# Optimization experiments

Hardware: AMD Instinct MI355X
Metric: run time of the kernel (lower is better)

## Reference

```python
import jax, jax.numpy as jnp
import numpy as np
import math

NUM_HEAD = 4
GROUPS = 32
EPS = 1e-5


def setup_inputs() -> dict:
    key = jax.random.key(0)
    k1, k2, k3 = jax.random.split(key, 3)
    B, C, H, W = 2, 256, 64, 64
    x = jax.random.normal(k1, (B, C, H, W), dtype=jnp.float32)
    gn_w = jnp.ones((C,), dtype=jnp.float32)
    gn_b = jnp.zeros((C,), dtype=jnp.float32)
    # scaling_init 'u' with scale=1: bound = sqrt(3*2/(fan_in+fan_out))
    fan = (C + 3 * C) / 2
    bound_qkv = math.sqrt(3.0 / fan)
    qkv_w = jax.random.uniform(k2, (3 * C, C), dtype=jnp.float32, minval=-bound_qkv, maxval=bound_qkv)
    bound_o = math.sqrt(3e-10 / C)
    o_w = jax.random.uniform(k3, (C, C), dtype=jnp.float32, minval=-bound_o, maxval=bound_o)
    o_b = jnp.zeros((C,), dtype=jnp.float32)
    return {"x": x, "gn_w": gn_w, "gn_b": gn_b, "qkv_w": qkv_w, "o_w": o_w, "o_b": o_b}


def _group_norm(x, w, b):
    B, C, H, W = x.shape
    xg = x.reshape(B, GROUPS, C // GROUPS, H, W)
    mean = xg.mean(axis=(2, 3, 4), keepdims=True)
    var = xg.var(axis=(2, 3, 4), keepdims=True)
    xn = ((xg - mean) * jax.lax.rsqrt(var + EPS)).reshape(B, C, H, W)
    return xn * w[None, :, None, None] + b[None, :, None, None]


def reference(x, gn_w, gn_b, qkv_w, o_w, o_b):
    B, C, H, W = x.shape
    hd = C // NUM_HEAD
    S = H * W
    norm = _group_norm(x, gn_w, gn_b)
    # 1x1 conv (no bias) == channel matmul
    qkv = jnp.einsum('oc,bchw->bohw', qkv_w, norm)
    qkv = qkv.reshape(B, NUM_HEAD, 3 * hd, S)
    q, k, v = jnp.split(qkv, 3, axis=2)  # each [B, nh, hd, S]
    scale = 1.0 / math.sqrt(C)  # note: sqrt(C), not sqrt(head_dim), per source
    attn = jnp.einsum('bncs,bnct->bnst', q, k) * scale  # [B, nh, S, S]
    attn = jax.nn.softmax(attn, axis=-1)
    out = jnp.einsum('bnst,bnct->bncs', attn, v).reshape(B, C, H, W)
    out = jnp.einsum('oc,bchw->bohw', o_w, out) + o_b[None, :, None, None]
    return out + x
```

## Files before the change

kernel.cpp:

```cpp
#include <hip/hip_runtime.h>
#include <hip/hip_bf16.h>

typedef __hip_bfloat16 bf16;
typedef short short8 __attribute__((ext_vector_type(8)));
typedef float f32x4 __attribute__((ext_vector_type(4)));

__device__ __forceinline__ float b2f(bf16 v) { return __bfloat162float(v); }

__device__ __forceinline__ unsigned short f2bf(float x) {
  unsigned u = __builtin_bit_cast(unsigned, x);
  unsigned r = u + 0x7fffu + ((u >> 16) & 1u);
  return (unsigned short)(r >> 16);
}
__device__ __forceinline__ unsigned pk2(float a, float b) {
  return (unsigned)f2bf(a) | ((unsigned)f2bf(b) << 16);
}
__device__ __forceinline__ unsigned pk2t(float a, float b) {
  return __builtin_amdgcn_perm(__builtin_bit_cast(unsigned, b),
                               __builtin_bit_cast(unsigned, a), 0x07060302u);
}
__device__ __forceinline__ float rd(const void* p, size_t i, int is32) {
  return is32 ? ((const float*)p)[i] : b2f(((const bf16*)p)[i]);
}
__device__ __forceinline__ float blo(unsigned w) {
  return __builtin_bit_cast(float, w << 16);
}
__device__ __forceinline__ float bhi(unsigned w) {
  return __builtin_bit_cast(float, w & 0xffff0000u);
}
__device__ __forceinline__ float fexp2(float x) {
  return __builtin_amdgcn_exp2f(x);
}

#define CQ 0.09016844005556022f

__global__ void __launch_bounds__(256) detect_kernel(const void* __restrict__ x,
                                                     int* __restrict__ flag) {
  __shared__ int cnt[256];
  const bf16* xb = (const bf16*)x;
  int c = 0;
  for (int i = threadIdx.x; i < 4096; i += 256) {
    float v = fabsf(b2f(xb[2 * i]));
    if (v >= 0.0009765625f && v <= 1024.0f) c++;
  }
  cnt[threadIdx.x] = c;
  __syncthreads();
  for (int off = 128; off > 0; off >>= 1) {
    if (threadIdx.x < off) cnt[threadIdx.x] += cnt[threadIdx.x + off];
    __syncthreads();
  }
  if (threadIdx.x == 0) *flag = (cnt[0] < 2048) ? 1 : 0;
}

__global__ void __launch_bounds__(256) pre1_kernel(
    const void* __restrict__ x, const void* __restrict__ gn_w,
    const void* __restrict__ gn_b, const int* __restrict__ flag,
    float* __restrict__ scale, float* __restrict__ shift,
    short* __restrict__ xT) {
  __shared__ __align__(16) float F[64][72];
  const int t = threadIdx.x;
  const int is32 = *flag;
  if (blockIdx.x < 512) {
    const int bx = blockIdx.x;
    const int b = bx >> 8, rest = bx & 255;
    const int s0 = (rest >> 2) * 64, c0 = (rest & 3) * 64;
    if (is32) {
      const float* xp = (const float*)x;
#pragma unroll
      for (int k = 0; k < 4; k++) {
        int idx = k * 256 + t, cl = idx >> 4, c4 = idx & 15;
        float4 v = *(const float4*)&xp[(size_t)(b * 256 + c0 + cl) * 4096 + s0 +
                                       c4 * 4];
        *(float4*)&F[cl][c4 * 4] = v;
      }
    } else {
      const bf16* xp = (const bf16*)x;
#pragma unroll
      for (int k = 0; k < 2; k++) {
        int idx = k * 256 + t, cl = idx >> 3, c8 = idx & 7;
        uint4 u = *(const uint4*)&xp[(size_t)(b * 256 + c0 + cl) * 4096 + s0 +
                                     c8 * 8];
        float4 f0, f1;
        f0.x = blo(u.x); f0.y = bhi(u.x); f0.z = blo(u.y); f0.w = bhi(u.y);
        f1.x = blo(u.z); f1.y = bhi(u.z); f1.z = blo(u.w); f1.w = bhi(u.w);
        *(float4*)&F[cl][c8 * 8] = f0;
        *(float4*)&F[cl][c8 * 8 + 4] = f1;
      }
    }
    __syncthreads();
#pragma unroll
    for (int k = 0; k < 8; k++) {
      int idx = k * 256 + t;
      int sl = idx >> 5, c2 = (idx & 31) * 2;
      unsigned u = pk2(F[c2][sl], F[c2 + 1][sl]);
      *(unsigned*)&xT[((size_t)b * 4096 + s0 + sl) * 256 + c0 + c2] = u;
    }
  } else {
    const int idx0 = blockIdx.x - 512;
    const int b = idx0 >> 5, g = idx0 & 31;
    const size_t base = (size_t)(b * 256 + g * 8) * 4096;
    float s = 0.f, ss = 0.f;
    if (is32) {
      const float4* p = (const float4*)((const float*)x + base);
      for (int i = t; i < 8192; i += 256) {
        float4 v = p[i];
        s += (v.x + v.y) + (v.z + v.w);
        ss += v.x * v.x + v.y * v.y + v.z * v.z + v.w * v.w;
      }
    } else {
      const uint4* p = (const uint4*)((const bf16*)x + base);
      for (int i = t; i < 4096; i += 256) {
        uint4 u = p[i];
#pragma unroll
        for (int k = 0; k < 4; k++) {
          unsigned w = (&u.x)[k];
          float lo = blo(w), hi = bhi(w);
          s += lo + hi;
          ss += lo * lo + hi * hi;
        }
      }
    }
    float* rs = &F[0][0];
    float* rq = rs + 256;
    rs[t] = s;
    rq[t] = ss;
    __syncthreads();
    for (int off = 128; off > 0; off >>= 1) {
      if (t < off) {
        rs[t] += rs[t + off];
        rq[t] += rq[t + off];
      }
      __syncthreads();
    }
    if (t < 8) {
      const float inv_n = 1.f / 32768.f;
      float mean = rs[0] * inv_n;
      float var = rq[0] * inv_n - mean * mean;
      float rstd = rsqrtf(var + 1e-5f);
      int c = g * 8 + t;
      float sc = rd(gn_w, c, is32) * rstd;
      scale[b * 256 + c] = sc;
      shift[b * 256 + c] = rd(gn_b, c, is32) - mean * sc;
    }
  }
}

__global__ void __launch_bounds__(256) pre2_kernel(
    const void* __restrict__ qkv_w, const void* __restrict__ o_w,
    const void* __restrict__ o_b, const float* __restrict__ scale,
    const float* __restrict__ shift, const int* __restrict__ flag,
    short* __restrict__ W2, float* __restrict__ bias2, short* __restrict__ owb,
    float* __restrict__ obf) {
  const int is32 = *flag;
  if (blockIdx.x < 192) {
    const int b = blockIdx.y;
    const int o = blockIdx.x * 4 + (threadIdx.x >> 6);
    const int lane = threadIdx.x & 63;
    const float f = (o % 192 < 64) ? CQ : 1.0f;
    float w[4], acc = 0.f;
#pragma unroll
    for (int k = 0; k < 4; k++) {
      int c = lane * 4 + k;
      w[k] = rd(qkv_w, (size_t)o * 256 + c, is32);
      acc += w[k] * shift[b * 256 + c];
      w[k] = w[k] * scale[b * 256 + c] * f;
    }
#pragma unroll
    for (int m = 1; m < 64; m <<= 1) acc += __shfl_xor(acc, m);
    if (lane == 0) bias2[b * 768 + o] = acc * f;
    uint2 u;
    u.x = pk2(w[0], w[1]);
    u.y = pk2(w[2], w[3]);
    *(uint2*)&W2[((size_t)b * 768 + o) * 256 + lane * 4] = u;
  } else if (blockIdx.y == 0) {
    int bx = blockIdx.x - 192;
    int i = (bx * 256 + threadIdx.x) * 4;
    uint2 u;
    u.x = pk2(rd(o_w, i, is32), rd(o_w, i + 1, is32));
    u.y = pk2(rd(o_w, i + 2, is32), rd(o_w, i + 3, is32));
    *(uint2*)&owb[i] = u;
    if (bx == 0) obf[threadIdx.x] = rd(o_b, threadIdx.x, is32);
  }
}

__global__ void __launch_bounds__(256) gemm_qkv_kernel(
    const short* __restrict__ xT, const short* __restrict__ W2,
    const float* __restrict__ bias2, short* __restrict__ qT,
    short* __restrict__ kF, short* __restrict__ vF) {
  __shared__ __align__(16) short lds[128 * 72 + 64 * 72];
  short* At = lds;
  short* Bt = lds + 128 * 72;
  const int t = threadIdx.x;
  const int wave = t >> 6, lane = t & 63;
  const int ln = lane & 15, quad = lane >> 4;
  const int s0 = blockIdx.x * 128, by = blockIdx.y, b = blockIdx.z;
  const int o0 = by * 64;
  const short* xg = xT + ((size_t)b * 4096 + s0) * 256;
  const short* wg = W2 + ((size_t)b * 768 + o0) * 256;

  f32x4 acc[2][4];
#pragma unroll
  for (int mt = 0; mt < 2; mt++)
#pragma unroll
    for (int nt = 0; nt < 4; nt++) {
      f32x4 z = {0.f, 0.f, 0.f, 0.f};
      acc[mt][nt] = z;
    }

  for (int kt = 0; kt < 4; kt++) {
    __syncthreads();
    {
      int r = t >> 1, ch = t & 1;
#pragma unroll
      for (int j = 0; j < 4; j++)
        *(uint4*)&At[r * 72 + ch * 32 + j * 8] =
            *(const uint4*)&xg[(size_t)r * 256 + kt * 64 + ch * 32 + j * 8];
    }
    {
      int r = t >> 2, cq = t & 3;
#pragma unroll
      for (int j = 0; j < 2; j++)
        *(uint4*)&Bt[r * 72 + cq * 16 + j * 8] =
            *(const uint4*)&wg[(size_t)r * 256 + kt * 64 + cq * 16 + j * 8];
    }
    __syncthreads();
#pragma unroll
    for (int kd = 0; kd < 2; kd++) {
      short8 a[2], bb[4];
#pragma unroll
      for (int mt = 0; mt < 2; mt++)
        a[mt] = *(const short8*)&At[(wave * 32 + mt * 16 + ln) * 72 + kd * 32 +
                                    quad * 8];
#pragma unroll
      for (int nt = 0; nt < 4; nt++)
        bb[nt] = *(const short8*)&Bt[(nt * 16 + ln) * 72 + kd * 32 + quad * 8];
#pragma unroll
      for (int mt = 0; mt < 2; mt++)
#pragma unroll
        for (int nt = 0; nt < 4; nt++)
          acc[mt][nt] = __builtin_amdgcn_mfma_f32_16x16x32_bf16(
              a[mt], bb[nt], acc[mt][nt], 0, 0, 0);
    }
  }

  const int h = by / 3, seg = by % 3;
  const size_t bh = (size_t)b * 4 + h;
  __syncthreads();
  if (seg != 2) {
    short* T = At;
#pragma unroll
    for (int mt = 0; mt < 2; mt++)
#pragma unroll
      for (int nt = 0; nt < 4; nt++)
#pragma unroll
        for (int r = 0; r < 4; r++)
          T[(wave * 32 + mt * 16 + quad * 4 + r) * 72 + nt * 16 + ln] =
              (short)f2bf(acc[mt][nt][r] + bias2[b * 768 + o0 + nt * 16 + ln]);
    __syncthreads();
    if (seg == 0) {
      short* dst = qT + (bh * 4096 + s0) * 64;
      int r = t >> 1, ch = t & 1;
#pragma unroll
      for (int j = 0; j < 2; j++)
        *(uint4*)&dst[r * 64 + ch * 32 + j * 8] =
            *(const uint4*)&T[r * 72 + ch * 32 + j * 8];
    } else {
      short* dstf = kF + bh * 262144;
#pragma unroll
      for (int c = 0; c < 4; c++) {
        int cid = wave * 4 + c;
        int tile = cid >> 1, kd = cid & 1;
        short8 v =
            *(const short8*)&T[(tile * 16 + ln) * 72 + kd * 32 + quad * 8];
        *(short8*)&dstf[(size_t)((s0 / 16 + tile) * 2 + kd) * 512 + lane * 8] =
            v;
      }
    }
  } else {
    short* T2 = At;
#pragma unroll
    for (int mt = 0; mt < 2; mt++)
#pragma unroll
      for (int nt = 0; nt < 4; nt++) {
        float bv = bias2[b * 768 + o0 + nt * 16 + ln];
        uint2 u;
        u.x = pk2(acc[mt][nt][0] + bv, acc[mt][nt][1] + bv);
        u.y = pk2(acc[mt][nt][2] + bv, acc[mt][nt][3] + bv);
        *(uint2*)&T2[(nt * 16 + ln) * 132 + wave * 32 + mt * 16 + quad * 4] = u;
      }
    __syncthreads();
    short* dstf = vF + bh * 262144;
#pragma unroll
    for (int c = 0; c < 4; c++) {
      int cid = wave * 4 + c;
      int ktl = cid >> 3, rem = cid & 7, dt = rem >> 1, kc = rem & 1;
      short8 v = *(const short8*)&T2[(dt * 16 + ln) * 132 + ktl * 64 + kc * 32 +
                                     quad * 8];
      *(short8*)&dstf[(size_t)(((s0 / 64 + ktl) * 4 + dt) * 2 + kc) * 512 +
                      lane * 8] = v;
    }
  }
}

__global__ void __launch_bounds__(256, 4) flash_kernel(
    const short* __restrict__ qT, const short* __restrict__ kF,
    const short* __restrict__ vF, short* __restrict__ attT) {
  __shared__ float smem[4 * 64 * 20];
  const int t = threadIdx.x;
  const int wave = t >> 6, lane = t & 63;
  const int ln = lane & 15, quad = lane >> 4;
  const int L = blockIdx.x;
  const int bh = L & 7;
  const int b = bh >> 2, h = bh & 3;
  const int q0 = (L >> 3) * 32;
  const int qt_sel = wave & 1;
  const int half = wave >> 1;

  const short* qg = qT + ((size_t)bh * 4096 + q0 + qt_sel * 16) * 64;
  const short* kf = kF + (size_t)bh * 262144 + (size_t)half * 131072;
  const short* vf = vF + (size_t)bh * 262144 + (size_t)half * 131072;

  short8 qf[2];
#pragma unroll
  for (int kd = 0; kd < 2; kd++)
    qf[kd] = *(const short8*)&qg[ln * 64 + kd * 32 + quad * 8];

  f32x4 ot[4];
#pragma unroll
  for (int dt = 0; dt < 4; dt++) {
    f32x4 z = {0.f, 0.f, 0.f, 0.f};
    ot[dt] = z;
  }
  float lres = 0.f;

  auto LOADKV = [&](short8(&ka)[2][2], short8(&va)[4], int it) {
    const short* kb = kf + (size_t)(it * 2) * 1024;
#pragma unroll
    for (int ct = 0; ct < 2; ct++)
#pragma unroll
      for (int kd = 0; kd < 2; kd++)
        ka[ct][kd] = *(const short8*)&kb[(ct * 2 + kd) * 512 + lane * 8];
    const short* vb = vf + (size_t)(it >> 1) * 4096;
    const int kc = it & 1;
#pragma unroll
    for (int dt = 0; dt < 4; dt++)
      va[dt] = *(const short8*)&vb[(dt * 2 + kc) * 512 + lane * 8];
  };

  auto STEP = [&](const short8(&ka)[2][2], const short8(&va)[4]) {
    f32x4 st[2];
#pragma unroll
    for (int ct = 0; ct < 2; ct++) {
      f32x4 z = {0.f, 0.f, 0.f, 0.f};
      st[ct] = z;
    }
#pragma unroll
    for (int kd = 0; kd < 2; kd++)
#pragma unroll
      for (int ct = 0; ct < 2; ct++)
        st[ct] = __builtin_amdgcn_mfma_f32_16x16x32_bf16(ka[ct][kd], qf[kd],
                                                         st[ct], 0, 0, 0);
    unsigned pk[2][2];
#pragma unroll
    for (int ct = 0; ct < 2; ct++) {
      float p0 = fexp2(st[ct][0]);
      float p1 = fexp2(st[ct][1]);
      float p2 = fexp2(st[ct][2]);
      float p3 = fexp2(st[ct][3]);
      lres += (p0 + p1) + (p2 + p3);
      pk[ct][0] = pk2t(p0, p1);
      pk[ct][1] = pk2t(p2, p3);
    }
    const int tt = quad >> 1;
    const int qs = (quad & 1) * 2;
    union {
      unsigned u[4];
      short8 s;
    } bu;
    bu.u[0] = (unsigned)__shfl((int)pk[tt][0], qs * 16 + ln);
    bu.u[1] = (unsigned)__shfl((int)pk[tt][1], qs * 16 + ln);
    bu.u[2] = (unsigned)__shfl((int)pk[tt][0], (qs + 1) * 16 + ln);
    bu.u[3] = (unsigned)__shfl((int)pk[tt][1], (qs + 1) * 16 + ln);
#pragma unroll
    for (int dt = 0; dt < 4; dt++)
      ot[dt] = __builtin_amdgcn_mfma_f32_16x16x32_bf16(va[dt], bu.s, ot[dt], 0,
                                                       0, 0);
  };

  short8 kaA[2][2], vaA[4], kaB[2][2], vaB[4];
  LOADKV(kaA, vaA, 0);
#pragma unroll 1
  for (int it = 0; it < 64; it += 2) {
    LOADKV(kaB, vaB, it + 1);
    STEP(kaA, vaA);
    if (it < 62) LOADKV(kaA, vaA, it + 2);
    STEP(kaB, vaB);
  }

  lres += __shfl_xor(lres, 16);
  lres += __shfl_xor(lres, 32);
  float* my = smem + (wave * 64 + lane) * 20;
#pragma unroll
  for (int dt = 0; dt < 4; dt++) *(f32x4*)&my[dt * 4] = ot[dt];
  my[16] = lres;
  __syncthreads();

  {
    const float* pA = smem + ((wave & 1) * 64 + lane) * 20;
    const float* pB = smem + (((wave & 1) + 2) * 64 + lane) * 20;
    float lf = pA[16] + pB[16];
    float invl = 1.f / lf;
    int s = q0 + (wave & 1) * 16 + ln;
    short* ap = attT + ((size_t)b * 4096 + s) * 256 + h * 64;
#pragma unroll
    for (int j = 0; j < 2; j++) {
      int dt = (wave >> 1) * 2 + j;
      f32x4 oA = *(const f32x4*)&pA[dt * 4];
      f32x4 oB = *(const f32x4*)&pB[dt * 4];
      uint2 u;
      u.x = pk2((oA[0] + oB[0]) * invl, (oA[1] + oB[1]) * invl);
      u.y = pk2((oA[2] + oB[2]) * invl, (oA[3] + oB[3]) * invl);
      *(uint2*)&ap[dt * 16 + quad * 4] = u;
    }
  }
}

__global__ void __launch_bounds__(256) gemm_o_kernel(
    const short* __restrict__ owb, const short* __restrict__ attT,
    const float* __restrict__ obf, const void* __restrict__ xres,
    void* __restrict__ out, const int* __restrict__ flag) {
  __shared__ __align__(16) float ldsf[64 * 66];
  short* Bt = (short*)ldsf;
  short* At = Bt + 64 * 72;
  const int t = threadIdx.x;
  const int wave = t >> 6, lane = t & 63;
  const int ln = lane & 15, quad = lane >> 4;
  const int s0 = blockIdx.x * 64, o0 = blockIdx.y * 64, b = blockIdx.z;
  const short* ag = attT + ((size_t)b * 4096 + s0) * 256;

  f32x4 acc[4];
#pragma unroll
  for (int mt = 0; mt < 4; mt++) {
    f32x4 z = {0.f, 0.f, 0.f, 0.f};
    acc[mt] = z;
  }

  for (int kt = 0; kt < 4; kt++) {
    __syncthreads();
    {
      int r = t >> 2, cq = t & 3;
#pragma unroll
      for (int j = 0; j < 2; j++)
        *(uint4*)&Bt[r * 72 + cq * 16 + j * 8] =
            *(const uint4*)&ag[(size_t)r * 256 + kt * 64 + cq * 16 + j * 8];
    }
    {
      int r = t >> 2, cq = t & 3;
#pragma unroll
      for (int j = 0; j < 2; j++)
        *(uint4*)&At[r * 72 + cq * 16 + j * 8] =
            *(const uint4*)&owb[(size_t)(o0 + r) * 256 + kt * 64 + cq * 16 +
                                j * 8];
    }
    __syncthreads();
#pragma unroll
    for (int kd = 0; kd < 2; kd++) {
      short8 a[4];
#pragma unroll
      for (int mt = 0; mt < 4; mt++)
        a[mt] = *(const short8*)&At[(mt * 16 + ln) * 72 + kd * 32 + quad * 8];
      short8 bb =
          *(const short8*)&Bt[(wave * 16 + ln) * 72 + kd * 32 + quad * 8];
#pragma unroll
      for (int mt = 0; mt < 4; mt++)
        acc[mt] = __builtin_amdgcn_mfma_f32_16x16x32_bf16(a[mt], bb, acc[mt],
                                                          0, 0, 0);
    }
  }

  __syncthreads();
#pragma unroll
  for (int mt = 0; mt < 4; mt++)
#pragma unroll
    for (int r = 0; r < 4; r++)
      ldsf[(mt * 16 + quad * 4 + r) * 66 + wave * 16 + ln] = acc[mt][r];
  __syncthreads();

  const int is32 = *flag;
#pragma unroll
  for (int j = 0; j < 4; j++) {
    int ol = j * 16 + (t >> 4);
    int sl = (t & 15) * 4;
    f32x4 v = *(const f32x4*)&ldsf[ol * 66 + sl];
    int o = o0 + ol;
    float bv = obf[o];
    size_t base = ((size_t)b * 256 + o) * 4096 + s0 + sl;
    if (is32) {
      const float4 rr = *(const float4*)&((const float*)xres)[base];
      float4 w;
      w.x = v[0] + bv + rr.x;
      w.y = v[1] + bv + rr.y;
      w.z = v[2] + bv + rr.z;
      w.w = v[3] + bv + rr.w;
      *(float4*)&((float*)out)[base] = w;
    } else {
      const uint2 rr = *(const uint2*)&((const bf16*)xres)[base];
      uint2 w;
      w.x = pk2(v[0] + bv + blo(rr.x), v[1] + bv + bhi(rr.x));
      w.y = pk2(v[2] + bv + blo(rr.y), v[3] + bv + bhi(rr.y));
      *(uint2*)&((bf16*)out)[base] = w;
    }
  }
}

extern "C" void kernel_launch(void* const* d_in, const int* in_sizes, int n_in,
                              void* d_out, int out_size, void* d_ws,
                              size_t ws_size, hipStream_t stream) {
  float* ws = (float*)d_ws;
  int* flag = (int*)ws;
  float* scale = ws + 256;
  float* shift = ws + 768;
  float* bias2 = ws + 1280;
  float* obf = ws + 2816;
  short* owb = (short*)(ws + 3072);
  short* W2 = (short*)(ws + 35840);
  short* xT = (short*)(ws + 232448);
  short* qT = (short*)(ws + 1281024);
  short* kF = (short*)(ws + 2329600);
  short* vF = (short*)(ws + 3378176);
  short* attT = (short*)(ws + 4426752);

  detect_kernel<<<1, 256, 0, stream>>>(d_in[0], flag);
  pre1_kernel<<<576, 256, 0, stream>>>(d_in[0], d_in[1], d_in[2], flag, scale,
                                       shift, xT);
  pre2_kernel<<<dim3(256, 2), 256, 0, stream>>>(d_in[3], d_in[4], d_in[5],
                                                scale, shift, flag, W2, bias2,
                                                owb, obf);
  gemm_qkv_kernel<<<dim3(32, 12, 2), 256, 0, stream>>>(xT, W2, bias2, qT, kF,
                                                       vF);
  flash_kernel<<<1024, 256, 0, stream>>>(qT, kF, vF, attT);
  gemm_o_kernel<<<dim3(64, 4, 2), 256, 0, stream>>>(owb, attT, obf, d_in[0],
                                                    d_out, flag);
}
```

Baseline: 172.7 us.

## Split KV across all four waves and reuse each K/V fragment for two query tiles

Each wave now handles both 16-row query tiles and a quarter of the key sequence, where before it handled one query tile and half the keys. Every loaded K/V fragment feeds two query tiles, which halves global K/V traffic per block and gives more MFMA work per load. The cost is more accumulator registers, a larger shared-memory reduction buffer (8 partial slices) and a four-way final combine, which may reduce occupancy at the launch bound of 4 blocks.

After: 161.1 us (median of 2 runs). -6.7%, faster.

```diff
diff --git a/kernel.cpp b/kernel.cpp
--- a/kernel.cpp
+++ b/kernel.cpp
@@ -305,7 +305,7 @@
 __global__ void __launch_bounds__(256, 4) flash_kernel(
     const short* __restrict__ qT, const short* __restrict__ kF,
     const short* __restrict__ vF, short* __restrict__ attT) {
-  __shared__ float smem[4 * 64 * 20];
+  __shared__ float smem[8 * 64 * 20];
   const int t = threadIdx.x;
   const int wave = t >> 6, lane = t & 63;
   const int ln = lane & 15, quad = lane >> 4;
@@ -313,33 +313,37 @@
   const int bh = L & 7;
   const int b = bh >> 2, h = bh & 3;
   const int q0 = (L >> 3) * 32;
-  const int qt_sel = wave & 1;
-  const int half = wave >> 1;
-
-  const short* qg = qT + ((size_t)bh * 4096 + q0 + qt_sel * 16) * 64;
-  const short* kf = kF + (size_t)bh * 262144 + (size_t)half * 131072;
-  const short* vf = vF + (size_t)bh * 262144 + (size_t)half * 131072;
-
-  short8 qf[2];
-#pragma unroll
-  for (int kd = 0; kd < 2; kd++)
-    qf[kd] = *(const short8*)&qg[ln * 64 + kd * 32 + quad * 8];
-
-  f32x4 ot[4];
-#pragma unroll
-  for (int dt = 0; dt < 4; dt++) {
-    f32x4 z = {0.f, 0.f, 0.f, 0.f};
-    ot[dt] = z;
-  }
-  float lres = 0.f;
-
-  auto LOADKV = [&](short8(&ka)[2][2], short8(&va)[4], int it) {
+
+  const short* qg = qT + ((size_t)bh * 4096 + q0) * 64;
+  const short* kf = kF + (size_t)bh * 262144 + (size_t)wave * 65536;
+  const short* vf = vF + (size_t)bh * 262144 + (size_t)wave * 65536;
+
+  short8 qf[2][2];
+#pragma unroll
+  for (int tq = 0; tq < 2; tq++)
+#pragma unroll
+    for (int kd = 0; kd < 2; kd++)
+      qf[tq][kd] = *(const short8*)&qg[(tq * 16 + ln) * 64 + kd * 32 + quad * 8];
+
+  f32x4 ot[2][4];
+#pragma unroll
+  for (int tq = 0; tq < 2; tq++)
+#pragma unroll
+    for (int dt = 0; dt < 4; dt++) {
+      f32x4 z = {0.f, 0.f, 0.f, 0.f};
+      ot[tq][dt] = z;
+    }
+  float lres[2] = {0.f, 0.f};
+
+  auto LOADK = [&](short8(&ka)[2][2], int it) {
     const short* kb = kf + (size_t)(it * 2) * 1024;
 #pragma unroll
     for (int ct = 0; ct < 2; ct++)
 #pragma unroll
       for (int kd = 0; kd < 2; kd++)
         ka[ct][kd] = *(const short8*)&kb[(ct * 2 + kd) * 512 + lane * 8];
+  };
+  auto LOADV = [&](short8(&va)[4], int it) {
     const short* vb = vf + (size_t)(it >> 1) * 4096;
     const int kc = it & 1;
 #pragma unroll
@@ -348,78 +352,94 @@
   };
 
   auto STEP = [&](const short8(&ka)[2][2], const short8(&va)[4]) {
-    f32x4 st[2];
-#pragma unroll
-    for (int ct = 0; ct < 2; ct++) {
-      f32x4 z = {0.f, 0.f, 0.f, 0.f};
-      st[ct] = z;
-    }
-#pragma unroll
-    for (int kd = 0; kd < 2; kd++)
-#pragma unroll
-      for (int ct = 0; ct < 2; ct++)
-        st[ct] = __builtin_amdgcn_mfma_f32_16x16x32_bf16(ka[ct][kd], qf[kd],
-                                                         st[ct], 0, 0, 0);
-    unsigned pk[2][2];
-#pragma unroll
-    for (int ct = 0; ct < 2; ct++) {
-      float p0 = fexp2(st[ct][0]);
-      float p1 = fexp2(st[ct][1]);
-      float p2 = fexp2(st[ct][2]);
-      float p3 = fexp2(st[ct][3]);
-      lres += (p0 + p1) + (p2 + p3);
-      pk[ct][0] = pk2t(p0, p1);
-      pk[ct][1] = pk2t(p2, p3);
-    }
-    const int tt = quad >> 1;
-    const int qs = (quad & 1) * 2;
-    union {
-      unsigned u[4];
-      short8 s;
-    } bu;
-    bu.u[0] = (unsigned)__shfl((int)pk[tt][0], qs * 16 + ln);
-    bu.u[1] = (unsigned)__shfl((int)pk[tt][1], qs * 16 + ln);
-    bu.u[2] = (unsigned)__shfl((int)pk[tt][0], (qs + 1) * 16 + ln);
-    bu.u[3] = (unsigned)__shfl((int)pk[tt][1], (qs + 1) * 16 + ln);
-#pragma unroll
-    for (int dt = 0; dt < 4; dt++)
-      ot[dt] = __builtin_amdgcn_mfma_f32_16x16x32_bf16(va[dt], bu.s, ot[dt], 0,
-                                                       0, 0);
+#pragma unroll
+    for (int tq = 0; tq < 2; tq++) {
+      f32x4 st[2];
+#pragma unroll
+      for (int ct = 0; ct < 2; ct++) {
+        f32x4 z = {0.f, 0.f, 0.f, 0.f};
+        st[ct] = z;
+      }
+#pragma unroll
+      for (int kd = 0; kd < 2; kd++)
+#pragma unroll
+        for (int ct = 0; ct < 2; ct++)
+          st[ct] = __builtin_amdgcn_mfma_f32_16x16x32_bf16(
+              ka[ct][kd], qf[tq][kd], st[ct], 0, 0, 0);
+      unsigned pk[2][2];
+#pragma unroll
+      for (int ct = 0; ct < 2; ct++) {
+        float p0 = fexp2(st[ct][0]);
+        float p1 = fexp2(st[ct][1]);
+        float p2 = fexp2(st[ct][2]);
+        float p3 = fexp2(st[ct][3]);
+        lres[tq] += (p0 + p1) + (p2 + p3);
+        pk[ct][0] = pk2t(p0, p1);
+        pk[ct][1] = pk2t(p2, p3);
+      }
+      const int tt = quad >> 1;
+      const int qs = (quad & 1) * 2;
+      union {
+        unsigned u[4];
+        short8 s;
+      } bu;
+      bu.u[0] = (unsigned)__shfl((int)pk[tt][0], qs * 16 + ln);
+      bu.u[1] = (unsigned)__shfl((int)pk[tt][1], qs * 16 + ln);
+      bu.u[2] = (unsigned)__shfl((int)pk[tt][0], (qs + 1) * 16 + ln);
+      bu.u[3] = (unsigned)__shfl((int)pk[tt][1], (qs + 1) * 16 + ln);
+#pragma unroll
+      for (int dt = 0; dt < 4; dt++)
+        ot[tq][dt] = __builtin_amdgcn_mfma_f32_16x16x32_bf16(
+            va[dt], bu.s, ot[tq][dt], 0, 0, 0);
+    }
   };
 
-  short8 kaA[2][2], vaA[4], kaB[2][2], vaB[4];
-  LOADKV(kaA, vaA, 0);
+  short8 kaA[2][2], kaB[2][2], va[4];
+  LOADK(kaA, 0);
 #pragma unroll 1
-  for (int it = 0; it < 64; it += 2) {
-    LOADKV(kaB, vaB, it + 1);
-    STEP(kaA, vaA);
-    if (it < 62) LOADKV(kaA, vaA, it + 2);
-    STEP(kaB, vaB);
-  }
-
-  lres += __shfl_xor(lres, 16);
-  lres += __shfl_xor(lres, 32);
-  float* my = smem + (wave * 64 + lane) * 20;
-#pragma unroll
-  for (int dt = 0; dt < 4; dt++) *(f32x4*)&my[dt * 4] = ot[dt];
-  my[16] = lres;
+  for (int it = 0; it < 32; it += 2) {
+    LOADV(va, it);
+    LOADK(kaB, it + 1);
+    STEP(kaA, va);
+    LOADV(va, it + 1);
+    if (it < 30) LOADK(kaA, it + 2);
+    STEP(kaB, va);
+  }
+
+#pragma unroll
+  for (int tq = 0; tq < 2; tq++) {
+    float l = lres[tq];
+    l += __shfl_xor(l, 16);
+    l += __shfl_xor(l, 32);
+    float* my = smem + ((wave * 2 + tq) * 64 + lane) * 20;
+#pragma unroll
+    for (int dt = 0; dt < 4; dt++) *(f32x4*)&my[dt * 4] = ot[tq][dt];
+    my[16] = l;
+  }
   __syncthreads();
 
   {
-    const float* pA = smem + ((wave & 1) * 64 + lane) * 20;
-    const float* pB = smem + (((wave & 1) + 2) * 64 + lane) * 20;
-    float lf = pA[16] + pB[16];
+    const int tq = wave & 1;
+    const float* p0 = smem + ((0 * 2 + tq) * 64 + lane) * 20;
+    const float* p1 = smem + ((1 * 2 + tq) * 64 + lane) * 20;
+    const float* p2 = smem + ((2 * 2 + tq) * 64 + lane) * 20;
+    const float* p3 = smem + ((3 * 2 + tq) * 64 + lane) * 20;
+    float lf = (p0[16] + p1[16]) + (p2[16] + p3[16]);
     float invl = 1.f / lf;
-    int s = q0 + (wave & 1) * 16 + ln;
+    int s = q0 + tq * 16 + ln;
     short* ap = attT + ((size_t)b * 4096 + s) * 256 + h * 64;
 #pragma unroll
     for (int j = 0; j < 2; j++) {
       int dt = (wave >> 1) * 2 + j;
-      f32x4 oA = *(const f32x4*)&pA[dt * 4];
-      f32x4 oB = *(const f32x4*)&pB[dt * 4];
+      f32x4 o0 = *(const f32x4*)&p0[dt * 4];
+      f32x4 o1 = *(const f32x4*)&p1[dt * 4];
+      f32x4 o2 = *(const f32x4*)&p2[dt * 4];
+      f32x4 o3 = *(const f32x4*)&p3[dt * 4];
       uint2 u;
-      u.x = pk2((oA[0] + oB[0]) * invl, (oA[1] + oB[1]) * invl);
-      u.y = pk2((oA[2] + oB[2]) * invl, (oA[3] + oB[3]) * invl);
+      u.x = pk2(((o0[0] + o1[0]) + (o2[0] + o3[0])) * invl,
+                ((o0[1] + o1[1]) + (o2[1] + o3[1])) * invl);
+      u.y = pk2(((o0[2] + o1[2]) + (o2[2] + o3[2])) * invl,
+                ((o0[3] + o1[3]) + (o2[3] + o3[3])) * invl);
       *(uint2*)&ap[dt * 16 + quad * 4] = u;
     }
   }
```

## Stage K/V tiles in LDS via async global-to-LDS loads shared by four waves

Applied to the files above, without the earlier changes.

The flash kernel now has each block handle 64 query rows, one 16-row tile per wave. All four waves share K/V tiles that are double-buffered in LDS and filled with global_load_lds direct copies. Previously each wave streamed its own half of K/V straight from global memory into registers, and a cross-wave reduction merged the partial outputs. The change cuts global K/V traffic and removes that final LDS reduction. In exchange it adds a block-wide barrier per key tile, halves the grid to 512 blocks, and lowers the occupancy hint to 2.

Result: faster. 166.7 us (-3.5%).

```diff
diff --git a/kernel.cpp b/kernel.cpp
--- a/kernel.cpp
+++ b/kernel.cpp
@@ -30,6 +30,11 @@
 }
 __device__ __forceinline__ float fexp2(float x) {
   return __builtin_amdgcn_exp2f(x);
+}
+__device__ __forceinline__ void gld_lds16(const void* g, void* l) {
+  __builtin_amdgcn_global_load_lds(
+      (const __attribute__((address_space(1))) unsigned int*)g,
+      (__attribute__((address_space(3))) unsigned int*)l, 16, 0, 0);
 }
 
 #define CQ 0.09016844005556022f
@@ -302,23 +307,21 @@
   }
 }
 
-__global__ void __launch_bounds__(256, 4) flash_kernel(
+__global__ void __launch_bounds__(256, 2) flash_kernel(
     const short* __restrict__ qT, const short* __restrict__ kF,
     const short* __restrict__ vF, short* __restrict__ attT) {
-  __shared__ float smem[4 * 64 * 20];
+  __shared__ __align__(16) short KV[2][8192];
   const int t = threadIdx.x;
   const int wave = t >> 6, lane = t & 63;
   const int ln = lane & 15, quad = lane >> 4;
   const int L = blockIdx.x;
   const int bh = L & 7;
   const int b = bh >> 2, h = bh & 3;
-  const int q0 = (L >> 3) * 32;
-  const int qt_sel = wave & 1;
-  const int half = wave >> 1;
-
-  const short* qg = qT + ((size_t)bh * 4096 + q0 + qt_sel * 16) * 64;
-  const short* kf = kF + (size_t)bh * 262144 + (size_t)half * 131072;
-  const short* vf = vF + (size_t)bh * 262144 + (size_t)half * 131072;
+  const int q0 = (L >> 3) * 64;
+
+  const short* qg = qT + ((size_t)bh * 4096 + q0 + wave * 16) * 64;
+  const short* kf = kF + (size_t)bh * 262144;
+  const short* vf = vF + (size_t)bh * 262144;
 
   short8 qf[2];
 #pragma unroll
@@ -333,21 +336,31 @@
   }
   float lres = 0.f;
 
-  auto LOADKV = [&](short8(&ka)[2][2], short8(&va)[4], int it) {
-    const short* kb = kf + (size_t)(it * 2) * 1024;
+  auto STAGE = [&](int bu, int kt) {
+    const short* ks = kf + (size_t)kt * 4096;
+    const short* vs = vf + (size_t)kt * 4096;
+#pragma unroll
+    for (int j = 0; j < 2; j++) {
+      gld_lds16(&ks[wave * 1024 + j * 512 + lane * 8],
+                &KV[bu][wave * 1024 + j * 512]);
+      gld_lds16(&vs[wave * 1024 + j * 512 + lane * 8],
+                &KV[bu][4096 + wave * 1024 + j * 512]);
+    }
+  };
+
+  auto STEP = [&](int bu, int s32) {
+    short8 ka[2][2], va[4];
 #pragma unroll
     for (int ct = 0; ct < 2; ct++)
 #pragma unroll
       for (int kd = 0; kd < 2; kd++)
-        ka[ct][kd] = *(const short8*)&kb[(ct * 2 + kd) * 512 + lane * 8];
-    const short* vb = vf + (size_t)(it >> 1) * 4096;
-    const int kc = it & 1;
+        ka[ct][kd] = *(const short8*)&KV[bu][((s32 * 2 + ct) * 2 + kd) * 512 +
+                                            lane * 8];
 #pragma unroll
     for (int dt = 0; dt < 4; dt++)
-      va[dt] = *(const short8*)&vb[(dt * 2 + kc) * 512 + lane * 8];
-  };
-
-  auto STEP = [&](const short8(&ka)[2][2], const short8(&va)[4]) {
+      va[dt] =
+          *(const short8*)&KV[bu][4096 + (dt * 2 + s32) * 512 + lane * 8];
+
     f32x4 st[2];
 #pragma unroll
     for (int ct = 0; ct < 2; ct++) {
@@ -376,52 +389,41 @@
     union {
       unsigned u[4];
       short8 s;
-    } bu;
-    bu.u[0] = (unsigned)__shfl((int)pk[tt][0], qs * 16 + ln);
-    bu.u[1] = (unsigned)__shfl((int)pk[tt][1], qs * 16 + ln);
-    bu.u[2] = (unsigned)__shfl((int)pk[tt][0], (qs + 1) * 16 + ln);
-    bu.u[3] = (unsigned)__shfl((int)pk[tt][1], (qs + 1) * 16 + ln);
+    } pu;
+    pu.u[0] = (unsigned)__shfl((int)pk[tt][0], qs * 16 + ln);
+    pu.u[1] = (unsigned)__shfl((int)pk[tt][1], qs * 16 + ln);
+    pu.u[2] = (unsigned)__shfl((int)pk[tt][0], (qs + 1) * 16 + ln);
+    pu.u[3] = (unsigned)__shfl((int)pk[tt][1], (qs + 1) * 16 + ln);
 #pragma unroll
     for (int dt = 0; dt < 4; dt++)
-      ot[dt] = __builtin_amdgcn_mfma_f32_16x16x32_bf16(va[dt], bu.s, ot[dt], 0,
-                                                       0, 0);
+      ot[dt] = __builtin_amdgcn_mfma_f32_16x16x32_bf16(va[dt], pu.s, ot[dt],
+                                                       0, 0, 0);
   };
 
-  short8 kaA[2][2], vaA[4], kaB[2][2], vaB[4];
-  LOADKV(kaA, vaA, 0);
+  STAGE(0, 0);
+  asm volatile("s_waitcnt vmcnt(0)" ::: "memory");
+  __syncthreads();
 #pragma unroll 1
-  for (int it = 0; it < 64; it += 2) {
-    LOADKV(kaB, vaB, it + 1);
-    STEP(kaA, vaA);
-    if (it < 62) LOADKV(kaA, vaA, it + 2);
-    STEP(kaB, vaB);
+  for (int kt = 0; kt < 64; kt++) {
+    const int cur = kt & 1;
+    if (kt < 63) STAGE(cur ^ 1, kt + 1);
+    STEP(cur, 0);
+    STEP(cur, 1);
+    asm volatile("s_waitcnt vmcnt(0)" ::: "memory");
+    __syncthreads();
   }
 
   lres += __shfl_xor(lres, 16);
   lres += __shfl_xor(lres, 32);
-  float* my = smem + (wave * 64 + lane) * 20;
-#pragma unroll
-  for (int dt = 0; dt < 4; dt++) *(f32x4*)&my[dt * 4] = ot[dt];
-  my[16] = lres;
-  __syncthreads();
-
-  {
-    const float* pA = smem + ((wave & 1) * 64 + lane) * 20;
-    const float* pB = smem + (((wave & 1) + 2) * 64 + lane) * 20;
-    float lf = pA[16] + pB[16];
-    float invl = 1.f / lf;
-    int s = q0 + (wave & 1) * 16 + ln;
-    short* ap = attT + ((size_t)b * 4096 + s) * 256 + h * 64;
-#pragma unroll
-    for (int j = 0; j < 2; j++) {
-      int dt = (wave >> 1) * 2 + j;
-      f32x4 oA = *(const f32x4*)&pA[dt * 4];
-      f32x4 oB = *(const f32x4*)&pB[dt * 4];
-      uint2 u;
-      u.x = pk2((oA[0] + oB[0]) * invl, (oA[1] + oB[1]) * invl);
-      u.y = pk2((oA[2] + oB[2]) * invl, (oA[3] + oB[3]) * invl);
-      *(uint2*)&ap[dt * 16 + quad * 4] = u;
-    }
+  float invl = 1.f / lres;
+  int s = q0 + wave * 16 + ln;
+  short* ap = attT + ((size_t)b * 4096 + s) * 256 + h * 64;
+#pragma unroll
+  for (int dt = 0; dt < 4; dt++) {
+    uint2 u;
+    u.x = pk2(ot[dt][0] * invl, ot[dt][1] * invl);
+    u.y = pk2(ot[dt][2] * invl, ot[dt][3] * invl);
+    *(uint2*)&ap[dt * 16 + quad * 4] = u;
   }
 }
 
@@ -538,7 +540,7 @@
                                                 owb, obf);
   gemm_qkv_kernel<<<dim3(32, 12, 2), 256, 0, stream>>>(xT, W2, bias2, qT, kF,
                                                        vF);
-  flash_kernel<<<1024, 256, 0, stream>>>(qT, kF, vF, attT);
+  flash_kernel<<<512, 256, 0, stream>>>(qT, kF, vF, attT);
   gemm_o_kernel<<<dim3(64, 4, 2), 256, 0, stream>>>(owb, attT, obf, d_in[0],
                                                     d_out, flag);
 }
```
